# Kernel optimization log

Measured on AMD Instinct MI355X. Metric: run time of the kernel, lower is better.

The kernel has to match this reference:

```python
import jax, jax.numpy as jnp
import numpy as np

B, S, D, H, FF = 2, 2048, 1024, 16, 4096
HD = D // H
SCALE = 1.0 / np.sqrt(HD).astype(np.float32)
EPS = 1e-5


def _ln(x, g, b):
    m = jnp.mean(x, axis=-1, keepdims=True)
    v = jnp.mean((x - m) ** 2, axis=-1, keepdims=True)
    return (x - m) * jax.lax.rsqrt(v + EPS) * g + b


def setup_inputs() -> dict:
    key = jax.random.key(0)
    ks = jax.random.split(key, 8)
    def lin(k, fan_in, shape):
        return (jax.random.normal(k, shape, jnp.float32) / np.sqrt(fan_in)).astype(jnp.float32)
    return {
        "x": jax.random.normal(ks[0], (B, S, D), jnp.float32),
        "w_qkv": lin(ks[1], D, (D, 3 * D)),          # qkv_proj (no bias)
        "w_o": lin(ks[2], D, (D, D)),                 # out_proj
        "b_o": jnp.zeros((D,), jnp.float32),
        "g1": jnp.ones((D,), jnp.float32),            # attn LayerNorm
        "bt1": jnp.zeros((D,), jnp.float32),
        "w1": lin(ks[3], D, (D, FF)),                 # FFN linear1
        "b1": jnp.zeros((FF,), jnp.float32),
        "w2": lin(ks[4], FF, (FF, D)),                # FFN linear2
        "b2": jnp.zeros((D,), jnp.float32),
        "g2": jnp.ones((D,), jnp.float32),            # FFN LayerNorm
        "bt2": jnp.zeros((D,), jnp.float32),
    }


def reference(x, w_qkv, w_o, b_o, g1, bt1, w1, b1, w2, b2, g2, bt2):
    # --- MultiHeadAttention (post-LN, dropout=eval/identity) ---
    qkv = (x @ w_qkv).reshape(B, S, H, 3 * HD)
    q, k, v = jnp.split(qkv, 3, axis=-1)  # each [B,S,H,HD]
    # kernel_func = scaled softmax over keys
    scores = jnp.einsum("bihd,bjhd->bhij", q, k) * SCALE  # [B,H,S,S]
    attn = jax.nn.softmax(scores, axis=-1)
    ao = jnp.einsum("bhij,bjhd->bihd", attn, v).reshape(B, S, D)
    y = _ln(x + ao @ w_o + b_o, g1, bt1)
    # --- FFN (post-LN) ---
    h = jax.nn.relu(y @ w1 + b1)
    return _ln(y + h @ w2 + b2, g2, bt2)
```

## Files before the change

### kernel.cpp

```cpp
#include <hip/hip_runtime.h>
#include <hip/hip_bf16.h>

#define B_  2
#define S_  2048
#define D_  1024
#define H_  16
#define HD_ 64
#define FF_ 4096
#define NT  (B_ * S_)
#define SCALE_ 0.125f
#define KLOG2E 0.1803368801111f
#define EPS_  1e-5f

typedef __attribute__((ext_vector_type(8))) short bf16x8;
typedef __attribute__((ext_vector_type(4))) float f32x4;

__device__ inline short f2bf(float f) {
    __hip_bfloat16 h = __float2bfloat16(f);
    return __builtin_bit_cast(short, h);
}
__device__ inline float bf2f(unsigned short u) {
    __hip_bfloat16 h = __builtin_bit_cast(__hip_bfloat16, u);
    return __bfloat162float(h);
}
__device__ inline unsigned int pk2bf(float lo, float hi) {
    __hip_bfloat162 h = __float22bfloat162_rn(float2{lo, hi});
    const unsigned short l16 = __builtin_bit_cast(unsigned short, h.x);
    const unsigned short h16 = __builtin_bit_cast(unsigned short, h.y);
    return (unsigned int)l16 | ((unsigned int)h16 << 16);
}

#define GLOBAL_AS __attribute__((address_space(1)))
#define LDS_AS    __attribute__((address_space(3)))

struct DetectArgs { const unsigned short* p[12]; int n[12]; };

__global__ __launch_bounds__(256) void detect_kernel(DetectArgs a, int* flags) {
    const int t = blockIdx.x;
    const unsigned short* s = a.p[t];
    const int cnt = min(a.n[t], 16384);
    const int tid = threadIdx.x;
    int huge = 0, zeven = 0;
    for (int i = tid; i < cnt; i += 256) {
        const unsigned short v = s[i];
        const int e = (v >> 7) & 0xFF;
        if (e >= 142) huge++;
        if (((i & 1) == 0) && ((v & 0x7FFF) == 0)) zeven++;
    }
    __shared__ int sh, sz;
    if (tid == 0) { sh = 0; sz = 0; }
    __syncthreads();
    atomicAdd(&sh, huge);
    atomicAdd(&sz, zeven);
    __syncthreads();
    if (tid == 0) flags[t] = (sh > 0 || sz * 4 > cnt) ? 1 : 0;
}

struct VecArgs { const void* src[7]; float* dst[7]; int n[7]; int fidx[7]; };

__global__ __launch_bounds__(256) void conv_x_vecs_kernel(
    const void* __restrict__ src, unsigned short* __restrict__ dst, int n,
    VecArgs a, const int* __restrict__ flags)
{
    const int i = blockIdx.x * 256 + threadIdx.x;
    if (i < n) {
        if (flags[0])
            dst[i] = (unsigned short)f2bf(((const float*)src)[i]);
        else
            dst[i] = ((const unsigned short*)src)[i];
    }
    if (blockIdx.x < 7) {
        const int v = blockIdx.x;
        const int f = flags[a.fidx[v]];
        for (int j = threadIdx.x; j < a.n[v]; j += 256) {
            a.dst[v][j] = f ? ((const float*)a.src[v])[j]
                            : bf2f(((const unsigned short*)a.src[v])[j]);
        }
    }
}

struct TArgs {
    const void* src[4]; unsigned short* dst[4];
    int K[4], N[4], fidx[4], start[5];
};

__global__ __launch_bounds__(256) void conv_t_all_kernel(
    TArgs t, const int* __restrict__ flags)
{
    __shared__ short T[32][33];
    const int tile = blockIdx.x;
    int w = 0;
    if (tile >= t.start[1]) w = 1;
    if (tile >= t.start[2]) w = 2;
    if (tile >= t.start[3]) w = 3;
    const int rel = tile - t.start[w];
    const int K = t.K[w], N = t.N[w];
    const int tilesN = N / 32;
    const int kt = (rel / tilesN) * 32, nt = (rel % tilesN) * 32;
    const void* src = t.src[w];
    unsigned short* dst = t.dst[w];
    const int f = flags[t.fidx[w]];

    const int c  = threadIdx.x & 31;
    const int r0 = (threadIdx.x >> 5) * 4;
#pragma unroll
    for (int i = 0; i < 4; i++) {
        const int r = r0 + i;
        const size_t gi = (size_t)(kt + r) * N + nt + c;
        short v = f ? f2bf(((const float*)src)[gi])
                    : (short)((const unsigned short*)src)[gi];
        T[c][r] = v;
    }
    __syncthreads();
#pragma unroll
    for (int i = 0; i < 4; i++) {
        const int n = r0 + i;
        dst[(size_t)(nt + n) * K + kt + c] = (unsigned short)T[n][c];
    }
}

#define G256_STAGE(tile_)                                                     \
    do {                                                                      \
        char* sb_ = smem + (size_t)((tile_) & 3) * 32768;                     \
        const int kb_ = (tile_) << 5;                                         \
        __builtin_amdgcn_global_load_lds(                                     \
            (const GLOBAL_AS void*)(ag0 + kb_),                               \
            (LDS_AS void*)(sb_ + sdst2), 16, 0, 0);                           \
        __builtin_amdgcn_global_load_lds(                                     \
            (const GLOBAL_AS void*)(ag1 + kb_),                               \
            (LDS_AS void*)(sb_ + 8192 + sdst2), 16, 0, 0);                    \
        __builtin_amdgcn_global_load_lds(                                     \
            (const GLOBAL_AS void*)(bg0 + kb_),                               \
            (LDS_AS void*)(sb_ + 16384 + sdst2), 16, 0, 0);                   \
        __builtin_amdgcn_global_load_lds(                                     \
            (const GLOBAL_AS void*)(bg1 + kb_),                               \
            (LDS_AS void*)(sb_ + 24576 + sdst2), 16, 0, 0);                   \
    } while (0)

template<bool HAS_BIAS, bool RELU, bool QSCALE>
__global__ __launch_bounds__(512) void gemm256_kernel(
    const unsigned short* __restrict__ A,
    const unsigned short* __restrict__ Bt,
    const float* __restrict__ bias,
    unsigned short* __restrict__ out,
    int M, int N, int K)
{
    extern __shared__ char smem[];

    const int tid  = threadIdx.x;
    const int wave = tid >> 6;
    const int lane = tid & 63;
    const int quad = lane >> 4;
    const int l16  = lane & 15;
    const int wr   = wave >> 2;
    const int wc   = wave & 3;

    const int row0 = blockIdx.x * 256;
    const int col0 = blockIdx.y * 256;

    const int srow  = tid >> 2;
    const int sk    = (((tid & 3) ^ ((srow >> 1) & 3)) * 8);
    const int sdst2 = srow * 64 + (tid & 3) * 16;
    const unsigned short* ag0 = A  + (size_t)(row0 + srow) * K + sk;
    const unsigned short* ag1 = A  + (size_t)(row0 + 128 + srow) * K + sk;
    const unsigned short* bg0 = Bt + (size_t)(col0 + srow) * K + sk;
    const unsigned short* bg1 = Bt + (size_t)(col0 + 128 + srow) * K + sk;

    const int rsw = (quad ^ ((l16 >> 1) & 3)) * 8;

    const int NTk = K >> 5;

    f32x4 acc[8][4] = {};

    G256_STAGE(0);
    G256_STAGE(1);
    G256_STAGE(2);

    for (int t = 0; t < NTk; t++) {
        if (t + 2 < NTk)
            asm volatile("s_waitcnt vmcnt(8)\n\ts_barrier" ::: "memory");
        else if (t + 1 < NTk)
            asm volatile("s_waitcnt vmcnt(4)\n\ts_barrier" ::: "memory");
        else
            asm volatile("s_waitcnt vmcnt(0)\n\ts_barrier" ::: "memory");

        const short* sA = (const short*)(smem + (size_t)(t & 3) * 32768);
        const short* sB = sA + 8192;

        bf16x8 af[8], bfr[4];
#pragma unroll
        for (int mi = 0; mi < 8; mi++)
            af[mi] = *reinterpret_cast<const bf16x8*>(
                &sA[(wr * 128 + mi * 16 + l16) * 32 + rsw]);
#pragma unroll
        for (int ni = 0; ni < 4; ni++)
            bfr[ni] = *reinterpret_cast<const bf16x8*>(
                &sB[(wc * 64 + ni * 16 + l16) * 32 + rsw]);
#pragma unroll
        for (int mi = 0; mi < 8; mi++)
#pragma unroll
            for (int ni = 0; ni < 4; ni++)
                acc[mi][ni] = __builtin_amdgcn_mfma_f32_16x16x32_bf16(
                    af[mi], bfr[ni], acc[mi][ni], 0, 0, 0);

        if (t + 3 < NTk) G256_STAGE(t + 3);
    }

#pragma unroll
    for (int ni = 0; ni < 4; ni++) {
        const int col = col0 + wc * 64 + ni * 16 + l16;
        float badd = 0.f;
        if constexpr (HAS_BIAS) badd = bias[col];
        float qs = 1.f;
        if constexpr (QSCALE)
            qs = (((col0 + wc * 64 + ni * 16) % 192) < 64) ? KLOG2E : 1.f;
#pragma unroll
        for (int mi = 0; mi < 8; mi++) {
#pragma unroll
            for (int r = 0; r < 4; r++) {
                const int row = row0 + wr * 128 + mi * 16 + quad * 4 + r;
                float v = acc[mi][ni][r] + badd;
                if constexpr (QSCALE) v *= qs;
                if constexpr (RELU) v = fmaxf(v, 0.f);
                out[(size_t)row * N + col] = (unsigned short)f2bf(v);
            }
        }
    }
}

__global__ __launch_bounds__(256) void gemm128_sk_kernel(
    const unsigned short* __restrict__ A,
    const unsigned short* __restrict__ Bt,
    float* __restrict__ out0,
    float* __restrict__ out1,
    int M, int N, int K)
{
    __shared__ short As[2][128 * 32];
    __shared__ short Bs[2][128 * 32];

    const int tid  = threadIdx.x;
    const int wave = tid >> 6;
    const int lane = tid & 63;
    const int quad = lane >> 4;
    const int l16  = lane & 15;

    const int row0 = blockIdx.x * 128;
    const int col0 = blockIdx.y * 128;
    const int z    = blockIdx.z;
    const int Kh   = K >> 1;

    const unsigned short* Az  = A  + (size_t)z * Kh;
    const unsigned short* Btz = Bt + (size_t)z * Kh;
    float* out = z ? out1 : out0;

    const int ldrow = lane >> 2;
    const int ldk   = (((lane & 3) ^ ((lane >> 3) & 3)) * 8);
    const unsigned short* agp0 = Az  + (size_t)(row0 + wave * 32 + ldrow) * K + ldk;
    const unsigned short* agp1 = agp0 + (size_t)16 * K;
    const unsigned short* bgp0 = Btz + (size_t)(col0 + wave * 32 + ldrow) * K + ldk;
    const unsigned short* bgp1 = bgp0 + (size_t)16 * K;

    const int wm = (wave >> 1) * 64;
    const int wn = (wave & 1) * 64;
    const int rsw = (quad ^ ((l16 >> 1) & 3)) * 8;

    f32x4 acc[4][4] = {};

#pragma unroll
    for (int h = 0; h < 2; h++) {
        __builtin_amdgcn_global_load_lds(
            (const GLOBAL_AS void*)(agp0 + h * 32),
            (LDS_AS void*)&As[h][wave * 1024 + lane * 8], 16, 0, 0);
        __builtin_amdgcn_global_load_lds(
            (const GLOBAL_AS void*)(agp1 + h * 32),
            (LDS_AS void*)&As[h][wave * 1024 + 512 + lane * 8], 16, 0, 0);
        __builtin_amdgcn_global_load_lds(
            (const GLOBAL_AS void*)(bgp0 + h * 32),
            (LDS_AS void*)&Bs[h][wave * 1024 + lane * 8], 16, 0, 0);
        __builtin_amdgcn_global_load_lds(
            (const GLOBAL_AS void*)(bgp1 + h * 32),
            (LDS_AS void*)&Bs[h][wave * 1024 + 512 + lane * 8], 16, 0, 0);
    }
    __syncthreads();

    for (int k0 = 0; k0 < Kh; k0 += 64) {
        const int kn = k0 + 64;
        const bool more = kn < Kh;
#pragma unroll
        for (int h = 0; h < 2; h++) {
            bf16x8 af[4], bfr[4];
#pragma unroll
            for (int mi = 0; mi < 4; mi++)
                af[mi] = *reinterpret_cast<const bf16x8*>(
                    &As[h][(wm + mi * 16 + l16) * 32 + rsw]);
#pragma unroll
            for (int ni = 0; ni < 4; ni++)
                bfr[ni] = *reinterpret_cast<const bf16x8*>(
                    &Bs[h][(wn + ni * 16 + l16) * 32 + rsw]);
#pragma unroll
            for (int mi = 0; mi < 4; mi++)
#pragma unroll
                for (int ni = 0; ni < 4; ni++)
                    acc[mi][ni] = __builtin_amdgcn_mfma_f32_16x16x32_bf16(
                        af[mi], bfr[ni], acc[mi][ni], 0, 0, 0);
            __syncthreads();
            if (more) {
                __builtin_amdgcn_global_load_lds(
                    (const GLOBAL_AS void*)(agp0 + kn + h * 32),
                    (LDS_AS void*)&As[h][wave * 1024 + lane * 8], 16, 0, 0);
                __builtin_amdgcn_global_load_lds(
                    (const GLOBAL_AS void*)(agp1 + kn + h * 32),
                    (LDS_AS void*)&As[h][wave * 1024 + 512 + lane * 8], 16, 0, 0);
                __builtin_amdgcn_global_load_lds(
                    (const GLOBAL_AS void*)(bgp0 + kn + h * 32),
                    (LDS_AS void*)&Bs[h][wave * 1024 + lane * 8], 16, 0, 0);
                __builtin_amdgcn_global_load_lds(
                    (const GLOBAL_AS void*)(bgp1 + kn + h * 32),
                    (LDS_AS void*)&Bs[h][wave * 1024 + 512 + lane * 8], 16, 0, 0);
            }
        }
    }

#pragma unroll
    for (int ni = 0; ni < 4; ni++) {
        const int col = col0 + wn + ni * 16 + l16;
#pragma unroll
        for (int mi = 0; mi < 4; mi++)
#pragma unroll
            for (int r = 0; r < 4; r++) {
                const int row = row0 + wm + mi * 16 + quad * 4 + r;
                out[(size_t)row * N + col] = acc[mi][ni][r];
            }
    }
}

__global__ __launch_bounds__(512) void attn_kernel(
    const unsigned short* __restrict__ qkv,
    unsigned short* __restrict__ ao)
{
    extern __shared__ char smem[];

    const int qt = blockIdx.x;
    const int h  = blockIdx.y;
    const int b  = blockIdx.z;

    const int tid  = threadIdx.x;
    const int wave = tid >> 6;
    const int g    = wave >> 2;
    const int gw   = wave & 3;
    const int lane = tid & 63;
    const int quad = lane >> 4;
    const int l16  = lane & 15;
    const int gtid = tid & 255;

    short* Ks = (short*)smem + g * (64 * 72);
    short* Vt = (short*)(smem + 18432) + g * (64 * 72);
    short* Ps = (short*)(smem + 36864) + wave * (32 * 72);

    bf16x8 qf[2][2];
#pragma unroll
    for (int mi = 0; mi < 2; mi++) {
        const int qrow = qt * 128 + gw * 32 + mi * 16 + l16;
        const unsigned short* qb = qkv + (size_t)(b * S_ + qrow) * 3072 + h * 192;
        qf[mi][0] = *reinterpret_cast<const bf16x8*>(qb + quad * 8);
        qf[mi][1] = *reinterpret_cast<const bf16x8*>(qb + 32 + quad * 8);
    }

    bf16x8 vones;
#pragma unroll
    for (int j = 0; j < 8; j++) vones[j] = (short)0x3F80;

    f32x4 o[2][4] = {};
    f32x4 o_l[2] = {};

    const int skey = gtid >> 3;
    const int soct = gtid & 7;
    const int vp   = gtid >> 3;
    const int kA   = (vp & 15) + ((vp >> 4) << 5);
    const int kB   = kA + 16;
    const int posA = 4 * (vp & 15) + 2 * (vp >> 4);
    const int vwr  = ((posA >> 3) ^ soct) * 8 + (posA & 7);

    const int kb0   = g * (S_ / 2);
    const int kbend = kb0 + S_ / 2;

    const unsigned short* kbase0 = qkv + (size_t)(b * S_) * 3072 + h * 192 + 64;
    const unsigned short* vbase0 = qkv + (size_t)(b * S_) * 3072 + h * 192 + 128;

    bf16x8 pk0 = *reinterpret_cast<const bf16x8*>(kbase0 + (size_t)(kb0 + skey) * 3072 + soct * 8);
    bf16x8 pk1 = *reinterpret_cast<const bf16x8*>(kbase0 + (size_t)(kb0 + skey + 32) * 3072 + soct * 8);
    bf16x8 pv0 = *reinterpret_cast<const bf16x8*>(vbase0 + (size_t)(kb0 + kA) * 3072 + soct * 8);
    bf16x8 pv1 = *reinterpret_cast<const bf16x8*>(vbase0 + (size_t)(kb0 + kB) * 3072 + soct * 8);

    for (int kb = kb0; kb < kbend; kb += 64) {
        {
            const int woct0 = soct ^ ((skey >> 3) & 1);
            *reinterpret_cast<bf16x8*>(&Ks[skey * 72 + woct0 * 8]) = pk0;
            const int woct1 = soct ^ (((skey + 32) >> 3) & 1);
            *reinterpret_cast<bf16x8*>(&Ks[(skey + 32) * 72 + woct1 * 8]) = pk1;
#pragma unroll
            for (int j = 0; j < 8; j++) {
                const int d = soct * 8 + j;
                const unsigned int val =
                    (unsigned int)(unsigned short)pv0[j] |
                    ((unsigned int)(unsigned short)pv1[j] << 16);
                *reinterpret_cast<unsigned int*>(&Vt[d * 72 + vwr]) = val;
            }
        }
        __syncthreads();

        {
            const int kbn = (kb + 64 < kbend) ? kb + 64 : kb;
            pk0 = *reinterpret_cast<const bf16x8*>(
                kbase0 + (size_t)(kbn + skey) * 3072 + soct * 8);
            pk1 = *reinterpret_cast<const bf16x8*>(
                kbase0 + (size_t)(kbn + skey + 32) * 3072 + soct * 8);
            pv0 = *reinterpret_cast<const bf16x8*>(
                vbase0 + (size_t)(kbn + kA) * 3072 + soct * 8);
            pv1 = *reinterpret_cast<const bf16x8*>(
                vbase0 + (size_t)(kbn + kB) * 3072 + soct * 8);
        }

        f32x4 s[2][4] = {};
#pragma unroll
        for (int c2 = 0; c2 < 2; c2++) {
#pragma unroll
            for (int nt = 0; nt < 4; nt++) {
                const int key = nt * 16 + l16;
                const int roct = (c2 * 4 + quad) ^ ((key >> 3) & 1);
                bf16x8 kf = *reinterpret_cast<const bf16x8*>(
                    &Ks[key * 72 + roct * 8]);
                s[0][nt] = __builtin_amdgcn_mfma_f32_16x16x32_bf16(qf[0][c2], kf, s[0][nt], 0, 0, 0);
                s[1][nt] = __builtin_amdgcn_mfma_f32_16x16x32_bf16(qf[1][c2], kf, s[1][nt], 0, 0, 0);
            }
        }

#pragma unroll
        for (int mi = 0; mi < 2; mi++) {
#pragma unroll
            for (int r = 0; r < 4; r++) {
                const int m = mi * 16 + quad * 4 + r;
                const float p0 = exp2f(s[mi][0][r]);
                const float p1 = exp2f(s[mi][1][r]);
                const float p2 = exp2f(s[mi][2][r]);
                const float p3 = exp2f(s[mi][3][r]);
                uint2 w;
                w.x = pk2bf(p0, p1);
                w.y = pk2bf(p2, p3);
                *reinterpret_cast<uint2*>(&Ps[m * 72 + l16 * 4]) = w;
            }
        }

#pragma unroll
        for (int c2 = 0; c2 < 2; c2++) {
            bf16x8 pf[2];
#pragma unroll
            for (int mi = 0; mi < 2; mi++) {
                const int m = mi * 16 + l16;
                pf[mi] = *reinterpret_cast<const bf16x8*>(
                    &Ps[m * 72 + c2 * 32 + quad * 8]);
            }
#pragma unroll
            for (int ct = 0; ct < 4; ct++) {
                const int row = ct * 16 + l16;
                const int blk = (c2 * 4 + quad) ^ (row >> 3);
                bf16x8 vf = *reinterpret_cast<const bf16x8*>(
                    &Vt[row * 72 + blk * 8]);
                o[0][ct] = __builtin_amdgcn_mfma_f32_16x16x32_bf16(pf[0], vf, o[0][ct], 0, 0, 0);
                o[1][ct] = __builtin_amdgcn_mfma_f32_16x16x32_bf16(pf[1], vf, o[1][ct], 0, 0, 0);
            }
            o_l[0] = __builtin_amdgcn_mfma_f32_16x16x32_bf16(pf[0], vones, o_l[0], 0, 0, 0);
            o_l[1] = __builtin_amdgcn_mfma_f32_16x16x32_bf16(pf[1], vones, o_l[1], 0, 0, 0);
        }
        __syncthreads();
    }

    float* ex = (float*)smem;
    const int slot = (gw * 64 + lane) * 40;
    if (g == 1) {
#pragma unroll
        for (int mi = 0; mi < 2; mi++) {
#pragma unroll
            for (int ct = 0; ct < 4; ct++)
                *reinterpret_cast<f32x4*>(&ex[slot + mi * 16 + ct * 4]) = o[mi][ct];
            *reinterpret_cast<f32x4*>(&ex[slot + 32 + mi * 4]) = o_l[mi];
        }
    }
    __syncthreads();
    if (g == 0) {
#pragma unroll
        for (int mi = 0; mi < 2; mi++) {
#pragma unroll
            for (int ct = 0; ct < 4; ct++) {
                f32x4 t = *reinterpret_cast<const f32x4*>(&ex[slot + mi * 16 + ct * 4]);
                o[mi][ct] += t;
            }
            f32x4 tl = *reinterpret_cast<const f32x4*>(&ex[slot + 32 + mi * 4]);
            o_l[mi] += tl;
        }
#pragma unroll
        for (int mi = 0; mi < 2; mi++) {
            f32x4 rl;
#pragma unroll
            for (int r = 0; r < 4; r++) rl[r] = 1.f / o_l[mi][r];
#pragma unroll
            for (int ct = 0; ct < 4; ct++)
#pragma unroll
                for (int r = 0; r < 4; r++) {
                    const int row = qt * 128 + gw * 32 + mi * 16 + quad * 4 + r;
                    ao[(size_t)(b * S_ + row) * D_ + h * HD_ + ct * 16 + l16] =
                        (unsigned short)f2bf(o[mi][ct][r] * rl[r]);
                }
        }
    }
}

template<int RESM, bool FLAG_OUT>
__global__ __launch_bounds__(256) void ln_sum_kernel(
    const float* __restrict__ p0,
    const float* __restrict__ p1,
    const float* __restrict__ bias,
    const unsigned short* __restrict__ resb,
    const float* __restrict__ resf,
    const float* __restrict__ g,
    const float* __restrict__ bt,
    const int* __restrict__ flags,
    void* __restrict__ out)
{
    const int row = blockIdx.x;
    const int tid = threadIdx.x;
    const int c0  = tid * 4;
    const size_t base = (size_t)row * D_ + c0;

    float4 a = *reinterpret_cast<const float4*>(p0 + base);
    float4 bq = *reinterpret_cast<const float4*>(p1 + base);
    float4 bi = *reinterpret_cast<const float4*>(bias + c0);

    float v[4] = {a.x + bq.x + bi.x, a.y + bq.y + bi.y,
                  a.z + bq.z + bi.z, a.w + bq.w + bi.w};

    if constexpr (RESM == 1) {
        if (flags[0]) {
            float4 rv = *reinterpret_cast<const float4*>(resf + base);
            v[0] += rv.x; v[1] += rv.y; v[2] += rv.z; v[3] += rv.w;
        } else {
            uint2 rv = *reinterpret_cast<const uint2*>(resb + base);
            v[0] += bf2f((unsigned short)(rv.x & 0xFFFF));
            v[1] += bf2f((unsigned short)(rv.x >> 16));
            v[2] += bf2f((unsigned short)(rv.y & 0xFFFF));
            v[3] += bf2f((unsigned short)(rv.y >> 16));
        }
    } else {
        uint2 rv = *reinterpret_cast<const uint2*>(resb + base);
        v[0] += bf2f((unsigned short)(rv.x & 0xFFFF));
        v[1] += bf2f((unsigned short)(rv.x >> 16));
        v[2] += bf2f((unsigned short)(rv.y & 0xFFFF));
        v[3] += bf2f((unsigned short)(rv.y >> 16));
    }

    float s = v[0] + v[1] + v[2] + v[3];
    float sq = v[0] * v[0] + v[1] * v[1] + v[2] * v[2] + v[3] * v[3];
#pragma unroll
    for (int msk = 1; msk < 64; msk <<= 1) {
        s += __shfl_xor(s, msk);
        sq += __shfl_xor(sq, msk);
    }
    __shared__ float ss[4], ssq[4];
    if ((tid & 63) == 0) { ss[tid >> 6] = s; ssq[tid >> 6] = sq; }
    __syncthreads();
    s = ss[0] + ss[1] + ss[2] + ss[3];
    sq = ssq[0] + ssq[1] + ssq[2] + ssq[3];

    const float mean = s * (1.f / D_);
    const float var = sq * (1.f / D_) - mean * mean;
    const float rinv = rsqrtf(var + EPS_);

    float w[4];
#pragma unroll
    for (int i = 0; i < 4; i++)
        w[i] = (v[i] - mean) * rinv * g[c0 + i] + bt[c0 + i];

    int outF32 = 0;
    if constexpr (FLAG_OUT) outF32 = flags[0];

    if (FLAG_OUT && outF32) {
        float4 o4 = {w[0], w[1], w[2], w[3]};
        *reinterpret_cast<float4*>((float*)out + base) = o4;
    } else {
        uint2 o2;
        o2.x = pk2bf(w[0], w[1]);
        o2.y = pk2bf(w[2], w[3]);
        *reinterpret_cast<uint2*>((unsigned short*)out + base) = o2;
    }
}

extern "C" void kernel_launch(void* const* d_in, const int* in_sizes, int n_in,
                              void* d_out, int out_size, void* d_ws, size_t ws_size,
                              hipStream_t stream) {
    char* ws = (char*)d_ws;

    int*            flags = (int*)(ws + 0);
    unsigned short* xb    = (unsigned short*)(ws + 256);
    unsigned short* wqkvT = (unsigned short*)(ws + 8388864);
    unsigned short* woT   = (unsigned short*)(ws + 14680320);
    unsigned short* w1T   = (unsigned short*)(ws + 16777472);
    unsigned short* w2T   = (unsigned short*)(ws + 25166080);
    float*          bof   = (float*)(ws + 33554688);
    float*          g1f   = (float*)(ws + 33558784);
    float*          bt1f  = (float*)(ws + 33562880);
    float*          b1f   = (float*)(ws + 33566976);
    float*          b2f   = (float*)(ws + 33583360);
    float*          g2f   = (float*)(ws + 33587456);
    float*          bt2f  = (float*)(ws + 33591552);
    unsigned short* qkv   = (unsigned short*)(ws + 33595648);
    unsigned short* ao    = (unsigned short*)(ws + 256);
    unsigned short* y     = (unsigned short*)(ws + 33595648);
    unsigned short* hbuf  = (unsigned short*)(ws + 41984256);
    float*          part0 = (float*)(ws + 58761472);
    float*          part1 = (float*)(ws + 75538688);
    float*          hpart0= (float*)(ws + 256);

    dim3 blk(256);

    static int attr_done = 0;
    if (!attr_done) {
        hipFuncSetAttribute(reinterpret_cast<const void*>(attn_kernel),
                            hipFuncAttributeMaxDynamicSharedMemorySize, 73728);
        hipFuncSetAttribute(
            reinterpret_cast<const void*>(&gemm256_kernel<false, false, true>),
            hipFuncAttributeMaxDynamicSharedMemorySize, 131072);
        hipFuncSetAttribute(
            reinterpret_cast<const void*>(&gemm256_kernel<true, true, false>),
            hipFuncAttributeMaxDynamicSharedMemorySize, 131072);
        attr_done = 1;
    }

    DetectArgs da;
    for (int i = 0; i < 12; i++) {
        da.p[i] = (const unsigned short*)d_in[i];
        da.n[i] = in_sizes[i];
    }
    detect_kernel<<<dim3(12), blk, 0, stream>>>(da, flags);

    VecArgs va;
    const int vidx[7] = {3, 4, 5, 7, 9, 10, 11};
    float* vdst[7] = {bof, g1f, bt1f, b1f, b2f, g2f, bt2f};
    for (int i = 0; i < 7; i++) {
        va.src[i] = d_in[vidx[i]];
        va.dst[i] = vdst[i];
        va.n[i]   = in_sizes[vidx[i]];
        va.fidx[i] = vidx[i];
    }
    conv_x_vecs_kernel<<<dim3((NT * D_ + 255) / 256), blk, 0, stream>>>(
        d_in[0], xb, NT * D_, va, flags);

    TArgs ta;
    ta.src[0] = d_in[1]; ta.dst[0] = wqkvT; ta.K[0] = D_;  ta.N[0] = 3 * D_; ta.fidx[0] = 1;
    ta.src[1] = d_in[2]; ta.dst[1] = woT;   ta.K[1] = D_;  ta.N[1] = D_;     ta.fidx[1] = 2;
    ta.src[2] = d_in[6]; ta.dst[2] = w1T;   ta.K[2] = D_;  ta.N[2] = FF_;    ta.fidx[2] = 6;
    ta.src[3] = d_in[8]; ta.dst[3] = w2T;   ta.K[3] = FF_; ta.N[3] = D_;     ta.fidx[3] = 8;
    ta.start[0] = 0;
    for (int wI = 0; wI < 4; wI++)
        ta.start[wI + 1] = ta.start[wI] + (ta.K[wI] / 32) * (ta.N[wI] / 32);
    conv_t_all_kernel<<<dim3(ta.start[4]), blk, 0, stream>>>(ta, flags);

    gemm256_kernel<false, false, true>
        <<<dim3(NT / 256, 3072 / 256), dim3(512), 131072, stream>>>(
            xb, wqkvT, nullptr, qkv, NT, 3072, 1024);

    attn_kernel<<<dim3(S_ / 128, H_, B_), dim3(512), 73728, stream>>>(qkv, ao);

    gemm128_sk_kernel<<<dim3(NT / 128, 1024 / 128, 2), blk, 0, stream>>>(
        ao, woT, part0, part1, NT, 1024, 1024);

    ln_sum_kernel<1, false><<<dim3(NT), blk, 0, stream>>>(
        part0, part1, bof, (const unsigned short*)d_in[0], (const float*)d_in[0],
        g1f, bt1f, flags, y);

    gemm256_kernel<true, true, false>
        <<<dim3(NT / 256, 4096 / 256), dim3(512), 131072, stream>>>(
            y, w1T, b1f, hbuf, NT, 4096, 1024);

    gemm128_sk_kernel<<<dim3(NT / 128, 1024 / 128, 2), blk, 0, stream>>>(
        hbuf, w2T, hpart0, part1, NT, 1024, 4096);

    ln_sum_kernel<2, true><<<dim3(NT), blk, 0, stream>>>(
        hpart0, part1, b2f, y, nullptr, g2f, bt2f, flags, d_out);
}
```

Baseline: 379.6 us.

## Deepen split-K GEMM pipeline to four-stage LDS ring with vmcnt waits

```diff
diff --git a/kernel.cpp b/kernel.cpp
--- a/kernel.cpp
+++ b/kernel.cpp
@@ -228,6 +228,24 @@
     }
 }
 
+#define GSK_STAGE(tile_)                                                      \
+    do {                                                                      \
+        char* sb_ = smem + (size_t)((tile_) & 3) * 16384;                     \
+        const int kb_ = (tile_) << 5;                                         \
+        __builtin_amdgcn_global_load_lds(                                     \
+            (const GLOBAL_AS void*)(agp0 + kb_),                              \
+            (LDS_AS void*)(sb_ + adst0), 16, 0, 0);                           \
+        __builtin_amdgcn_global_load_lds(                                     \
+            (const GLOBAL_AS void*)(agp1 + kb_),                              \
+            (LDS_AS void*)(sb_ + adst1), 16, 0, 0);                           \
+        __builtin_amdgcn_global_load_lds(                                     \
+            (const GLOBAL_AS void*)(bgp0 + kb_),                              \
+            (LDS_AS void*)(sb_ + 8192 + adst0), 16, 0, 0);                    \
+        __builtin_amdgcn_global_load_lds(                                     \
+            (const GLOBAL_AS void*)(bgp1 + kb_),                              \
+            (LDS_AS void*)(sb_ + 8192 + adst1), 16, 0, 0);                    \
+    } while (0)
+
 __global__ __launch_bounds__(256) void gemm128_sk_kernel(
     const unsigned short* __restrict__ A,
     const unsigned short* __restrict__ Bt,
@@ -235,8 +253,7 @@
     float* __restrict__ out1,
     int M, int N, int K)
 {
-    __shared__ short As[2][128 * 32];
-    __shared__ short Bs[2][128 * 32];
+    extern __shared__ char smem[];
 
     const int tid  = threadIdx.x;
     const int wave = tid >> 6;
@@ -254,71 +271,55 @@
     float* out = z ? out1 : out0;
 
     const int ldrow = lane >> 2;
-    const int ldk   = (((lane & 3) ^ ((lane >> 3) & 3)) * 8);
+    const int ldk   = (((lane & 3) ^ ((ldrow >> 1) & 3)) * 8);
     const unsigned short* agp0 = Az  + (size_t)(row0 + wave * 32 + ldrow) * K + ldk;
     const unsigned short* agp1 = agp0 + (size_t)16 * K;
     const unsigned short* bgp0 = Btz + (size_t)(col0 + wave * 32 + ldrow) * K + ldk;
     const unsigned short* bgp1 = bgp0 + (size_t)16 * K;
 
+    const int adst0 = (wave * 32 + ldrow) * 64 + (lane & 3) * 16;
+    const int adst1 = adst0 + 16 * 64;
+
     const int wm = (wave >> 1) * 64;
     const int wn = (wave & 1) * 64;
     const int rsw = (quad ^ ((l16 >> 1) & 3)) * 8;
 
+    const int NTk = Kh >> 5;
+
     f32x4 acc[4][4] = {};
 
-#pragma unroll
-    for (int h = 0; h < 2; h++) {
-        __builtin_amdgcn_global_load_lds(
-            (const GLOBAL_AS void*)(agp0 + h * 32),
-            (LDS_AS void*)&As[h][wave * 1024 + lane * 8], 16, 0, 0);
-        __builtin_amdgcn_global_load_lds(
-            (const GLOBAL_AS void*)(agp1 + h * 32),
-            (LDS_AS void*)&As[h][wave * 1024 + 512 + lane * 8], 16, 0, 0);
-        __builtin_amdgcn_global_load_lds(
-            (const GLOBAL_AS void*)(bgp0 + h * 32),
-            (LDS_AS void*)&Bs[h][wave * 1024 + lane * 8], 16, 0, 0);
-        __builtin_amdgcn_global_load_lds(
-            (const GLOBAL_AS void*)(bgp1 + h * 32),
-            (LDS_AS void*)&Bs[h][wave * 1024 + 512 + lane * 8], 16, 0, 0);
-    }
-    __syncthreads();
-
-    for (int k0 = 0; k0 < Kh; k0 += 64) {
-        const int kn = k0 + 64;
-        const bool more = kn < Kh;
-#pragma unroll
-        for (int h = 0; h < 2; h++) {
-            bf16x8 af[4], bfr[4];
-#pragma unroll
-            for (int mi = 0; mi < 4; mi++)
-                af[mi] = *reinterpret_cast<const bf16x8*>(
-                    &As[h][(wm + mi * 16 + l16) * 32 + rsw]);
+    GSK_STAGE(0);
+    if (1 < NTk) GSK_STAGE(1);
+    if (2 < NTk) GSK_STAGE(2);
+
+    for (int t = 0; t < NTk; t++) {
+        if (t + 2 < NTk)
+            asm volatile("s_waitcnt vmcnt(8)\n\ts_barrier" ::: "memory");
+        else if (t + 1 < NTk)
+            asm volatile("s_waitcnt vmcnt(4)\n\ts_barrier" ::: "memory");
+        else
+            asm volatile("s_waitcnt vmcnt(0)\n\ts_barrier" ::: "memory");
+
+        const short* sA = (const short*)(smem + (size_t)(t & 3) * 16384);
+        const short* sB = sA + 4096;
+
+        bf16x8 af[4], bfr[4];
+#pragma unroll
+        for (int mi = 0; mi < 4; mi++)
+            af[mi] = *reinterpret_cast<const bf16x8*>(
+                &sA[(wm + mi * 16 + l16) * 32 + rsw]);
+#pragma unroll
+        for (int ni = 0; ni < 4; ni++)
+            bfr[ni] = *reinterpret_cast<const bf16x8*>(
+                &sB[(wn + ni * 16 + l16) * 32 + rsw]);
+#pragma unroll
+        for (int mi = 0; mi < 4; mi++)
 #pragma unroll
             for (int ni = 0; ni < 4; ni++)
-                bfr[ni] = *reinterpret_cast<const bf16x8*>(
-                    &Bs[h][(wn + ni * 16 + l16) * 32 + rsw]);
-#pragma unroll
-            for (int mi = 0; mi < 4; mi++)
-#pragma unroll
-                for (int ni = 0; ni < 4; ni++)
-                    acc[mi][ni] = __builtin_amdgcn_mfma_f32_16x16x32_bf16(
-                        af[mi], bfr[ni], acc[mi][ni], 0, 0, 0);
-            __syncthreads();
-            if (more) {
-                __builtin_amdgcn_global_load_lds(
-                    (const GLOBAL_AS void*)(agp0 + kn + h * 32),
-                    (LDS_AS void*)&As[h][wave * 1024 + lane * 8], 16, 0, 0);
-                __builtin_amdgcn_global_load_lds(
-                    (const GLOBAL_AS void*)(agp1 + kn + h * 32),
-                    (LDS_AS void*)&As[h][wave * 1024 + 512 + lane * 8], 16, 0, 0);
-                __builtin_amdgcn_global_load_lds(
-                    (const GLOBAL_AS void*)(bgp0 + kn + h * 32),
-                    (LDS_AS void*)&Bs[h][wave * 1024 + lane * 8], 16, 0, 0);
-                __builtin_amdgcn_global_load_lds(
-                    (const GLOBAL_AS void*)(bgp1 + kn + h * 32),
-                    (LDS_AS void*)&Bs[h][wave * 1024 + 512 + lane * 8], 16, 0, 0);
-            }
-        }
+                acc[mi][ni] = __builtin_amdgcn_mfma_f32_16x16x32_bf16(
+                    af[mi], bfr[ni], acc[mi][ni], 0, 0, 0);
+
+        if (t + 3 < NTk) GSK_STAGE(t + 3);
     }
 
 #pragma unroll
@@ -632,6 +633,8 @@
         hipFuncSetAttribute(
             reinterpret_cast<const void*>(&gemm256_kernel<true, true, false>),
             hipFuncAttributeMaxDynamicSharedMemorySize, 131072);
+        hipFuncSetAttribute(reinterpret_cast<const void*>(gemm128_sk_kernel),
+                            hipFuncAttributeMaxDynamicSharedMemorySize, 65536);
         attr_done = 1;
     }
 
@@ -670,7 +673,7 @@
 
     attn_kernel<<<dim3(S_ / 128, H_, B_), dim3(512), 73728, stream>>>(qkv, ao);
 
-    gemm128_sk_kernel<<<dim3(NT / 128, 1024 / 128, 2), blk, 0, stream>>>(
+    gemm128_sk_kernel<<<dim3(NT / 128, 1024 / 128, 2), blk, 65536, stream>>>(
         ao, woT, part0, part1, NT, 1024, 1024);
 
     ln_sum_kernel<1, false><<<dim3(NT), blk, 0, stream>>>(
@@ -681,7 +684,7 @@
         <<<dim3(NT / 256, 4096 / 256), dim3(512), 131072, stream>>>(
             y, w1T, b1f, hbuf, NT, 4096, 1024);
 
-    gemm128_sk_kernel<<<dim3(NT / 128, 1024 / 128, 2), blk, 0, stream>>>(
+    gemm128_sk_kernel<<<dim3(NT / 128, 1024 / 128, 2), blk, 65536, stream>>>(
         hbuf, w2T, hpart0, part1, NT, 1024, 4096);
 
     ln_sum_kernel<2, true><<<dim3(NT), blk, 0, stream>>>(
```

Result: no change. 372.5 us, median of 2 (-1.9%).
